# Kernel tuning notes

Hardware: AMD Instinct MI355X
Metric: run time of the kernel (lower is better)

## Reference

```python
import jax, jax.numpy as jnp
import numpy as np

B, T = 32, 50
CONCEPT_NUM = 500
C = CONCEPT_NUM + 1          # self.concept_num = concept_num + 1
H, E = 32, 32                # hidden_dim, embedding_dim
BN_SCALE = 1.0 / np.sqrt(1.0 + 1e-5)  # eval-mode BatchNorm1d, default running stats


def _mlp(x, w1, b1, w2, b2):
    # MLP: relu(fc1) -> (dropout off in eval) -> relu(fc2) -> BatchNorm1d(eval)
    x = jax.nn.relu(x @ w1.T + b1)
    x = jax.nn.relu(x @ w2.T + b2)
    return x * BN_SCALE


def _gru(x, h, w_ih, w_hh, b_ih, b_hh):
    # torch.nn.GRUCell semantics; gate order r, z, n
    gx = x @ w_ih.T + b_ih
    gh = h @ w_hh.T + b_hh
    hd = h.shape[-1]
    r = jax.nn.sigmoid(gx[..., :hd] + gh[..., :hd])
    z = jax.nn.sigmoid(gx[..., hd:2 * hd] + gh[..., hd:2 * hd])
    n = jnp.tanh(gx[..., 2 * hd:] + r * gh[..., 2 * hd:])
    return (1.0 - z) * n + z * h


def setup_inputs() -> dict:
    key = jax.random.key(0)
    ks = jax.random.split(key, 32)
    HE = H + E
    def lin(k, out_d, in_d):
        return jax.random.normal(k, (out_d, in_d), jnp.float32) * (1.0 / np.sqrt(in_d))
    inp = {
        'features': jax.random.randint(ks[0], (B, T), 0, 2 * C, jnp.int64),
        'questions': jax.random.randint(ks[1], (B, T), 0, C, jnp.int64),
        'graph': jax.random.uniform(ks[2], (C, C), jnp.float32),
        'emb_x': jax.random.normal(ks[3], (2 * C, E), jnp.float32),
        'emb_c': jax.random.normal(ks[4], (C, E), jnp.float32),
        # f_self: MLP(H+E -> H -> H)
        'self_w1': lin(ks[5], H, HE), 'self_b1': jnp.full((H,), 0.1, jnp.float32),
        'self_w2': lin(ks[6], H, H),  'self_b2': jnp.full((H,), 0.1, jnp.float32),
        # f_neighbor_list[0]: MLP(2*(H+E) -> H -> H)
        'n0_w1': lin(ks[7], H, 2 * HE), 'n0_b1': jnp.full((H,), 0.1, jnp.float32),
        'n0_w2': lin(ks[8], H, H),      'n0_b2': jnp.full((H,), 0.1, jnp.float32),
        # f_neighbor_list[1]
        'n1_w1': lin(ks[9], H, 2 * HE),  'n1_b1': jnp.full((H,), 0.1, jnp.float32),
        'n1_w2': lin(ks[10], H, H),      'n1_b2': jnp.full((H,), 0.1, jnp.float32),
        # EraseAddGate
        'ea_w': jax.random.uniform(ks[11], (C,), jnp.float32, -1.0, 1.0) / np.sqrt(C),
        'ea_ew': lin(ks[12], H, H), 'ea_eb': jnp.zeros((H,), jnp.float32),
        'ea_aw': lin(ks[13], H, H), 'ea_ab': jnp.zeros((H,), jnp.float32),
        # GRUCell
        'gru_w_ih': lin(ks[14], 3 * H, H), 'gru_w_hh': lin(ks[15], 3 * H, H),
        'gru_b_ih': jnp.zeros((3 * H,), jnp.float32), 'gru_b_hh': jnp.zeros((3 * H,), jnp.float32),
        # predict
        'pred_w': lin(ks[16], 1, H), 'pred_b': jnp.zeros((1,), jnp.float32),
    }
    return inp


def reference(features, questions, graph, emb_x, emb_c,
              self_w1, self_b1, self_w2, self_b2,
              n0_w1, n0_b1, n0_w2, n0_b2,
              n1_w1, n1_b1, n1_w2, n1_b2,
              ea_w, ea_ew, ea_eb, ea_aw, ea_ab,
              gru_w_ih, gru_w_hh, gru_b_ih, gru_b_hh,
              pred_w, pred_b):
    b_ar = jnp.arange(B)

    def step(ht, inp):
        xt, qt = inp  # [B], [B]
        # _aggregate: response embedding via one_hot(xt) @ emb_x == gather
        res_emb = emb_x[xt]                                          # [B, E]
        ce = jnp.broadcast_to(emb_c[None], (B, C, E))                # [B, C, E]
        ce = ce.at[b_ar, qt].set(res_emb)
        tmp_ht = jnp.concatenate([ht, ce], axis=-1)                  # [B, C, H+E]
        # _agg_neighbors (Dense graph, 2 edge types)
        self_ht = tmp_ht[b_ar, qt]                                   # [B, H+E]
        self_feat = _mlp(self_ht, self_w1, self_b1, self_w2, self_b2)
        neigh_ht = jnp.concatenate(
            [jnp.broadcast_to(self_ht[:, None], tmp_ht.shape), tmp_ht], axis=-1)  # [B, C, 2(H+E)]
        adj = graph[qt][..., None]                                   # [B, C, 1]
        radj = graph[:, qt].T[..., None]                             # [B, C, 1]
        neigh = adj * _mlp(neigh_ht, n0_w1, n0_b1, n0_w2, n0_b2) \
              + radj * _mlp(neigh_ht, n1_w1, n1_b1, n1_w2, n1_b2)    # [B, C, H]
        m = neigh.at[b_ar, qt].set(self_feat)
        # EraseAddGate
        eg = jax.nn.sigmoid(m @ ea_ew.T + ea_eb)
        af = jnp.tanh(m @ ea_aw.T + ea_ab)
        w = ea_w[None, :, None]
        m = m - w * eg * m + w * af
        # GRUCell over every (student, concept)
        h_next = _gru(m.reshape(-1, H), ht.reshape(-1, H),
                      gru_w_ih, gru_w_hh, gru_b_ih, gru_b_hh).reshape(B, C, H)
        yt = jax.nn.sigmoid((h_next @ pred_w.T + pred_b)[..., 0])    # [B, C]
        return h_next, yt

    ht0 = jnp.zeros((B, C, H), dtype=graph.dtype)
    _, yts = jax.lax.scan(step, ht0, (features.T, questions.T))      # [T, B, C]
    # _get_next_pred: prediction for question at t+1 from state after step t
    yts = jnp.moveaxis(yts[:-1], 0, 1)                               # [B, T-1, C]
    q_next = questions[:, 1:]                                        # [B, T-1]
    pred = jnp.take_along_axis(yts, q_next[..., None], axis=-1)[..., 0]
    return pred                                                      # [B, T-1]
```

## Files before the change

kernel.cpp:

```cpp
#include <hip/hip_runtime.h>
#include <math.h>

#define BB 32
#define TT 50
#define CC 501
#define NNODES (BB*CC)
#define BN_SCALEF 0.9999950000374996f

#define V 4
#define NPW 8
#define WPB 8
#define NTH 512
#define NPB (NPW*WPB)
#define NBLK ((NNODES + NPB - 1)/NPB)

#define HT_SZ   (NNODES*32)
#define P_SZ    (CC*32)
#define GT_SZ   (CC*CC)
#define PERB_BUF (BB*96)

__device__ __forceinline__ float dot4(float4 a, float4 b){
    return a.x*b.x + a.y*b.y + a.z*b.z + a.w*b.w;
}
__device__ __forceinline__ float sigm(float x){ return 1.f/(1.f+__expf(-x)); }
__device__ __forceinline__ float tanhfast(float x){ return 1.f - 2.f/(__expf(2.f*x)+1.f); }

__global__ void init0_kernel(const float* __restrict__ graph,
                             float* __restrict__ graphT,
                             float* __restrict__ ht) {
    int i = blockIdx.x*blockDim.x + threadIdx.x;
    if (i < HT_SZ) ht[i] = 0.f;
    if (i < GT_SZ) {
        int r = i / CC, c2 = i % CC;
        graphT[i] = graph[c2*CC + r];
    }
}

__global__ void pk_kernel(const float* __restrict__ n0_w1, const float* __restrict__ n1_w1,
                          const float* __restrict__ emb_c,
                          float* __restrict__ P0, float* __restrict__ P1) {
    int c = blockIdx.x;
    int which = threadIdx.x >> 5, j = threadIdx.x & 31;
    float ec = emb_c[c*32 + j];
    const float* W = which ? n1_w1 : n0_w1;
    float acc = 0.f;
    #pragma unroll
    for (int k = 0; k < 32; k++)
        acc += W[j*128 + 96 + k] * __shfl(ec, k, 32);
    (which ? P1 : P0)[c*32 + j] = acc;
}

__global__ void perb0_kernel(const int* __restrict__ features, const float* __restrict__ emb_x,
                             const float* __restrict__ n0_w1, const float* __restrict__ n0_b1,
                             const float* __restrict__ n1_w1, const float* __restrict__ n1_b1,
                             const float* __restrict__ self_w1, const float* __restrict__ self_b1,
                             const float* __restrict__ self_w2, const float* __restrict__ self_b2,
                             float* __restrict__ perb) {
    int b = threadIdx.x >> 5, j = threadIdx.x & 31;
    int xt = features[b*TT + 0];
    float eq = emb_x[xt*32 + j];
    float a0 = n0_b1[j], a1 = n1_b1[j], s = self_b1[j];
    #pragma unroll
    for (int k = 0; k < 32; k++) {
        float ek = __shfl(eq, k, 32);
        a0 += n0_w1[j*128 + 32 + k] * ek;
        a1 += n1_w1[j*128 + 32 + k] * ek;
        s  += self_w1[j*64 + 32 + k] * ek;
    }
    float l1 = fmaxf(s, 0.f);
    float s2 = self_b2[j];
    #pragma unroll
    for (int k = 0; k < 32; k++) s2 += self_w2[j*32 + k] * __shfl(l1, k, 32);
    perb[b*96 + j]      = a0;
    perb[b*96 + 32 + j] = a1;
    perb[b*96 + 64 + j] = fmaxf(s2, 0.f) * BN_SCALEF;
}

__global__ __launch_bounds__(NTH, 1) void step_kernel(
    int t,
    const int* __restrict__ features, const int* __restrict__ questions,
    const float* __restrict__ graph,  const float* __restrict__ emb_x,
    const float* __restrict__ self_w1, const float* __restrict__ self_b1,
    const float* __restrict__ self_w2, const float* __restrict__ self_b2,
    const float* __restrict__ n0_w1, const float* __restrict__ n0_b1,
    const float* __restrict__ n0_w2, const float* __restrict__ n0_b2,
    const float* __restrict__ n1_w1, const float* __restrict__ n1_b1,
    const float* __restrict__ n1_w2, const float* __restrict__ n1_b2,
    const float* __restrict__ ea_w,  const float* __restrict__ ea_ew,
    const float* __restrict__ ea_eb, const float* __restrict__ ea_aw,
    const float* __restrict__ ea_ab,
    const float* __restrict__ gru_w_ih, const float* __restrict__ gru_w_hh,
    const float* __restrict__ gru_b_ih, const float* __restrict__ gru_b_hh,
    const float* __restrict__ pred_w,   const float* __restrict__ pred_b,
    float* __restrict__ ht,
    const float* __restrict__ P0, const float* __restrict__ P1,
    const float* __restrict__ graphT,
    float* __restrict__ perb, float* __restrict__ out)
{
    __shared__ float Wq[12288];
    __shared__ float xb[WPB][3][NPW][32];

    int tid = threadIdx.x;
    for (int idx = tid; idx < 12288; idx += NTH) {
        float v;
        if (idx < 6144) {
            int region = idx >> 10;
            int r = idx & 1023;
            int j = (r >> 2) & 31;
            int k = ((r >> 7) << 2) | (r & 3);
            switch (region) {
                case 0:  v = n0_w1[j*128 + 64 + k]; break;
                case 1:  v = n1_w1[j*128 + 64 + k]; break;
                case 2:  v = n0_w2[j*32 + k]; break;
                case 3:  v = n1_w2[j*32 + k]; break;
                case 4:  v = ea_ew[j*32 + k]; break;
                default: v = ea_aw[j*32 + k]; break;
            }
            Wq[idx] = v;
        } else {
            int r = idx - 6144;
            int which = r / 3072;
            int r2 = r % 3072;
            int row = (r2 >> 2) % 96;
            int k = ((r2 / 384) << 2) | (r2 & 3);
            Wq[idx] = which ? gru_w_hh[row*32 + k] : gru_w_ih[row*32 + k];
        }
    }

    int l   = tid & 63;
    int w   = tid >> 6;
    int j   = l & 31, sub = l >> 5;
    int nodebase = blockIdx.x*NPB + w*NPW;
    bool act = nodebase < NNODES;

    int bv[V], cv[V], qtv[V];
    float hj[V], adjv[V], radjv[V];
    if (act) {
        #pragma unroll
        for (int v = 0; v < V; v++) {
            int node = nodebase + 2*v + sub;
            int b = node / CC;
            int c = node - b*CC;
            bv[v] = b; cv[v] = c;
            int qt = questions[b*TT + t];
            qtv[v] = qt;
            adjv[v]  = graph [qt*CC + c];
            radjv[v] = graphT[qt*CC + c];
            float h = ht[node*32 + j];
            hj[v] = h;
            xb[w][0][2*v+sub][j] = h;
        }
    }
    __syncthreads();
    if (!act) return;

    int pbase = (t & 1)*PERB_BUF;

    {
        float acc0[V], acc1[V];
        #pragma unroll
        for (int v = 0; v < V; v++) {
            acc0[v] = perb[pbase + bv[v]*96 + j]      + P0[cv[v]*32 + j];
            acc1[v] = perb[pbase + bv[v]*96 + 32 + j] + P1[cv[v]*32 + j];
        }
        #pragma unroll
        for (int kc = 0; kc < 8; kc++) {
            float4 w0 = *(const float4*)&Wq[       kc*128 + j*4];
            float4 w1 = *(const float4*)&Wq[1024 + kc*128 + j*4];
            #pragma unroll
            for (int v = 0; v < V; v++) {
                float4 x = *(const float4*)&xb[w][0][2*v+sub][kc*4];
                acc0[v] += dot4(w0, x);
                acc1[v] += dot4(w1, x);
            }
        }
        #pragma unroll
        for (int v = 0; v < V; v++) {
            xb[w][1][2*v+sub][j] = fmaxf(acc0[v], 0.f);
            xb[w][2][2*v+sub][j] = fmaxf(acc1[v], 0.f);
        }
    }

    float mval[V];
    {
        float a0[V], a1[V];
        float b0 = n0_b2[j], b1 = n1_b2[j];
        #pragma unroll
        for (int v = 0; v < V; v++) { a0[v] = b0; a1[v] = b1; }
        #pragma unroll
        for (int kc = 0; kc < 8; kc++) {
            float4 w0 = *(const float4*)&Wq[2048 + kc*128 + j*4];
            float4 w1 = *(const float4*)&Wq[3072 + kc*128 + j*4];
            #pragma unroll
            for (int v = 0; v < V; v++) {
                float4 va = *(const float4*)&xb[w][1][2*v+sub][kc*4];
                float4 vb = *(const float4*)&xb[w][2][2*v+sub][kc*4];
                a0[v] += dot4(w0, va);
                a1[v] += dot4(w1, vb);
            }
        }
        #pragma unroll
        for (int v = 0; v < V; v++) {
            float f0 = fmaxf(a0[v], 0.f) * BN_SCALEF;
            float f1 = fmaxf(a1[v], 0.f) * BN_SCALEF;
            float m = adjv[v]*f0 + radjv[v]*f1;
            if (cv[v] == qtv[v]) m = perb[pbase + bv[v]*96 + 64 + j];
            mval[v] = m;
            xb[w][1][2*v+sub][j] = m;
        }
    }

    {
        float e[V], aa[V];
        float be = ea_eb[j], ba = ea_ab[j];
        #pragma unroll
        for (int v = 0; v < V; v++) { e[v] = be; aa[v] = ba; }
        #pragma unroll
        for (int kc = 0; kc < 8; kc++) {
            float4 we = *(const float4*)&Wq[4096 + kc*128 + j*4];
            float4 wa = *(const float4*)&Wq[5120 + kc*128 + j*4];
            #pragma unroll
            for (int v = 0; v < V; v++) {
                float4 vm = *(const float4*)&xb[w][1][2*v+sub][kc*4];
                e[v]  += dot4(we, vm);
                aa[v] += dot4(wa, vm);
            }
        }
        #pragma unroll
        for (int v = 0; v < V; v++) {
            float eg = sigm(e[v]);
            float af = tanhfast(aa[v]);
            float wc = ea_w[cv[v]];
            float m  = mval[v];
            xb[w][2][2*v+sub][j] = m - wc*eg*m + wc*af;
        }
    }

    float gh0[V], gh1[V], gh2[V];
    {
        float bh0 = gru_b_hh[j], bh1 = gru_b_hh[32+j], bh2 = gru_b_hh[64+j];
        #pragma unroll
        for (int v = 0; v < V; v++) { gh0[v]=bh0; gh1[v]=bh1; gh2[v]=bh2; }
        #pragma unroll
        for (int kc = 0; kc < 8; kc++) {
            const float* wh = &Wq[9216 + kc*384];
            float4 wh0 = *(const float4*)&wh[j*4];
            float4 wh1 = *(const float4*)&wh[(32+j)*4];
            float4 wh2 = *(const float4*)&wh[(64+j)*4];
            #pragma unroll
            for (int v = 0; v < V; v++) {
                float4 vh = *(const float4*)&xb[w][0][2*v+sub][kc*4];
                gh0[v] += dot4(wh0, vh);
                gh1[v] += dot4(wh1, vh);
                gh2[v] += dot4(wh2, vh);
            }
        }
    }
    float hn[V];
    {
        float gi0[V], gi1[V], gi2[V];
        float bi0 = gru_b_ih[j], bi1 = gru_b_ih[32+j], bi2 = gru_b_ih[64+j];
        #pragma unroll
        for (int v = 0; v < V; v++) { gi0[v]=bi0; gi1[v]=bi1; gi2[v]=bi2; }
        #pragma unroll
        for (int kc = 0; kc < 8; kc++) {
            const float* wi = &Wq[6144 + kc*384];
            float4 wi0 = *(const float4*)&wi[j*4];
            float4 wi1 = *(const float4*)&wi[(32+j)*4];
            float4 wi2 = *(const float4*)&wi[(64+j)*4];
            #pragma unroll
            for (int v = 0; v < V; v++) {
                float4 vm = *(const float4*)&xb[w][2][2*v+sub][kc*4];
                gi0[v] += dot4(wi0, vm);
                gi1[v] += dot4(wi1, vm);
                gi2[v] += dot4(wi2, vm);
            }
        }
        #pragma unroll
        for (int v = 0; v < V; v++) {
            float r = sigm(gi0[v] + gh0[v]);
            float z = sigm(gi1[v] + gh1[v]);
            float n = tanhfast(gi2[v] + r*gh2[v]);
            hn[v] = (1.f - z)*n + z*hj[v];
            int node = nodebase + 2*v + sub;
            ht[node*32 + j] = hn[v];
        }
    }

    #pragma unroll
    for (int v = 0; v < V; v++) {
        int qn = questions[bv[v]*TT + t + 1];
        if (cv[v] == qn) {
            float s = hn[v] * pred_w[j];
            #pragma unroll
            for (int off = 16; off; off >>= 1) s += __shfl_down(s, off, 32);
            if (j == 0) out[bv[v]*(TT-1) + t] = sigm(s + pred_b[0]);

            if (t < TT - 2) {
                int xt1 = features[bv[v]*TT + t + 1];
                float eq = emb_x[xt1*32 + j];
                float accA0 = n0_b1[j], accA1 = n1_b1[j], accS = self_b1[j];
                #pragma unroll
                for (int k = 0; k < 32; k++) {
                    float hk = __shfl(hn[v], k, 32);
                    float ek = __shfl(eq, k, 32);
                    accA0 += n0_w1[j*128 + k]*hk + n0_w1[j*128 + 32 + k]*ek;
                    accA1 += n1_w1[j*128 + k]*hk + n1_w1[j*128 + 32 + k]*ek;
                    accS  += self_w1[j*64 + k]*hk + self_w1[j*64 + 32 + k]*ek;
                }
                float l1 = fmaxf(accS, 0.f);
                float s2 = self_b2[j];
                #pragma unroll
                for (int k = 0; k < 32; k++) s2 += self_w2[j*32 + k] * __shfl(l1, k, 32);
                float* pn = perb + ((t+1) & 1)*PERB_BUF + bv[v]*96;
                pn[j]      = accA0;
                pn[32 + j] = accA1;
                pn[64 + j] = fmaxf(s2, 0.f) * BN_SCALEF;
            }
        }
    }
}

extern "C" void kernel_launch(void* const* d_in, const int* in_sizes, int n_in,
                              void* d_out, int out_size, void* d_ws, size_t ws_size,
                              hipStream_t stream) {
    const int*   features = (const int*)  d_in[0];
    const int*   questions= (const int*)  d_in[1];
    const float* graph    = (const float*)d_in[2];
    const float* emb_x    = (const float*)d_in[3];
    const float* emb_c    = (const float*)d_in[4];
    const float* self_w1  = (const float*)d_in[5];
    const float* self_b1  = (const float*)d_in[6];
    const float* self_w2  = (const float*)d_in[7];
    const float* self_b2  = (const float*)d_in[8];
    const float* n0_w1    = (const float*)d_in[9];
    const float* n0_b1    = (const float*)d_in[10];
    const float* n0_w2    = (const float*)d_in[11];
    const float* n0_b2    = (const float*)d_in[12];
    const float* n1_w1    = (const float*)d_in[13];
    const float* n1_b1    = (const float*)d_in[14];
    const float* n1_w2    = (const float*)d_in[15];
    const float* n1_b2    = (const float*)d_in[16];
    const float* ea_w     = (const float*)d_in[17];
    const float* ea_ew    = (const float*)d_in[18];
    const float* ea_eb    = (const float*)d_in[19];
    const float* ea_aw    = (const float*)d_in[20];
    const float* ea_ab    = (const float*)d_in[21];
    const float* gru_w_ih = (const float*)d_in[22];
    const float* gru_w_hh = (const float*)d_in[23];
    const float* gru_b_ih = (const float*)d_in[24];
    const float* gru_b_hh = (const float*)d_in[25];
    const float* pred_w   = (const float*)d_in[26];
    const float* pred_b   = (const float*)d_in[27];
    float* out = (float*)d_out;

    float* ws     = (float*)d_ws;
    float* ht     = ws;
    float* P0     = ht + HT_SZ;
    float* P1     = P0 + P_SZ;
    float* graphT = P1 + P_SZ;
    float* perb   = graphT + GT_SZ;

    init0_kernel<<<(HT_SZ + 255)/256, 256, 0, stream>>>(graph, graphT, ht);
    pk_kernel<<<CC, 64, 0, stream>>>(n0_w1, n1_w1, emb_c, P0, P1);
    perb0_kernel<<<1, 1024, 0, stream>>>(features, emb_x,
        n0_w1, n0_b1, n1_w1, n1_b1, self_w1, self_b1, self_w2, self_b2, perb);

    for (int t = 0; t < TT - 1; t++) {
        step_kernel<<<NBLK, NTH, 0, stream>>>(
            t, features, questions, graph, emb_x,
            self_w1, self_b1, self_w2, self_b2,
            n0_w1, n0_b1, n0_w2, n0_b2,
            n1_w1, n1_b1, n1_w2, n1_b2,
            ea_w, ea_ew, ea_eb, ea_aw, ea_ab,
            gru_w_ih, gru_w_hh, gru_b_ih, gru_b_hh,
            pred_w, pred_b,
            ht, P0, P1, graphT, perb, out);
    }
}
```

Before: 1.225 ms.

## Fuse all timesteps into one persistent kernel with grid-wide atomic barriers

Replaces the 49 per-timestep launches with a single persistent kernel of 251 blocks that loops over timesteps and synchronises through an atomic-counter grid barrier per step. Each block loads the shared-memory weight copy once and handles its nodes in two passes, so per-step launch overhead and repeated weight staging go away. GRU hidden-gate partials are staged in shared memory to cut register pressure. It relies on all 251 blocks being co-resident, and the spin barrier adds latency and a deadlock risk if they are not.

```diff
diff --git a/kernel.cpp b/kernel.cpp
--- a/kernel.cpp
+++ b/kernel.cpp
@@ -6,19 +6,32 @@
 #define CC 501
 #define NNODES (BB*CC)
 #define BN_SCALEF 0.9999950000374996f
+#define NSTEP (TT-1)
 
 #define V 4
-#define NPW 8
-#define WPB 8
-#define NTH 512
-#define NPB (NPW*WPB)
-#define NBLK ((NNODES + NPB - 1)/NPB)
+#define WPB 4
+#define NTH 256
+#define NPB 64
+#define NBLK 251
 
 #define HT_SZ   (NNODES*32)
 #define P_SZ    (CC*32)
 #define GT_SZ   (CC*CC)
 #define PERB_BUF (BB*96)
 
+struct Params {
+    const int* features; const int* questions;
+    const float* graph;  const float* emb_x;
+    const float* self_w1; const float* self_b1; const float* self_w2; const float* self_b2;
+    const float* n0_w1; const float* n0_b1; const float* n0_w2; const float* n0_b2;
+    const float* n1_w1; const float* n1_b1; const float* n1_w2; const float* n1_b2;
+    const float* ea_w; const float* ea_ew; const float* ea_eb; const float* ea_aw; const float* ea_ab;
+    const float* gru_w_ih; const float* gru_w_hh; const float* gru_b_ih; const float* gru_b_hh;
+    const float* pred_w; const float* pred_b;
+    float* ht; const float* P0; const float* P1; const float* graphT;
+    float* perb; float* out; unsigned* bar;
+};
+
 __device__ __forceinline__ float dot4(float4 a, float4 b){
     return a.x*b.x + a.y*b.y + a.z*b.z + a.w*b.w;
 }
@@ -27,13 +40,15 @@
 
 __global__ void init0_kernel(const float* __restrict__ graph,
                              float* __restrict__ graphT,
-                             float* __restrict__ ht) {
+                             float* __restrict__ ht,
+                             unsigned* __restrict__ bar) {
     int i = blockIdx.x*blockDim.x + threadIdx.x;
     if (i < HT_SZ) ht[i] = 0.f;
     if (i < GT_SZ) {
         int r = i / CC, c2 = i % CC;
         graphT[i] = graph[c2*CC + r];
     }
+    if (i < 64) bar[i] = 0u;
 }
 
 __global__ void pk_kernel(const float* __restrict__ n0_w1, const float* __restrict__ n1_w1,
@@ -76,29 +91,23 @@
     perb[b*96 + 64 + j] = fmaxf(s2, 0.f) * BN_SCALEF;
 }
 
-__global__ __launch_bounds__(NTH, 1) void step_kernel(
-    int t,
-    const int* __restrict__ features, const int* __restrict__ questions,
-    const float* __restrict__ graph,  const float* __restrict__ emb_x,
-    const float* __restrict__ self_w1, const float* __restrict__ self_b1,
-    const float* __restrict__ self_w2, const float* __restrict__ self_b2,
-    const float* __restrict__ n0_w1, const float* __restrict__ n0_b1,
-    const float* __restrict__ n0_w2, const float* __restrict__ n0_b2,
-    const float* __restrict__ n1_w1, const float* __restrict__ n1_b1,
-    const float* __restrict__ n1_w2, const float* __restrict__ n1_b2,
-    const float* __restrict__ ea_w,  const float* __restrict__ ea_ew,
-    const float* __restrict__ ea_eb, const float* __restrict__ ea_aw,
-    const float* __restrict__ ea_ab,
-    const float* __restrict__ gru_w_ih, const float* __restrict__ gru_w_hh,
-    const float* __restrict__ gru_b_ih, const float* __restrict__ gru_b_hh,
-    const float* __restrict__ pred_w,   const float* __restrict__ pred_b,
-    float* __restrict__ ht,
-    const float* __restrict__ P0, const float* __restrict__ P1,
-    const float* __restrict__ graphT,
-    float* __restrict__ perb, float* __restrict__ out)
-{
+__device__ __forceinline__ void gbar(unsigned* ctr) {
+    __builtin_amdgcn_fence(__ATOMIC_RELEASE, "agent");
+    __syncthreads();
+    if (threadIdx.x == 0) {
+        __hip_atomic_fetch_add(ctr, 1u, __ATOMIC_RELAXED, __HIP_MEMORY_SCOPE_AGENT);
+        while (__hip_atomic_load(ctr, __ATOMIC_RELAXED, __HIP_MEMORY_SCOPE_AGENT) < (unsigned)NBLK) {
+            __builtin_amdgcn_s_sleep(2);
+        }
+    }
+    __syncthreads();
+    __builtin_amdgcn_fence(__ATOMIC_ACQUIRE, "agent");
+}
+
+__global__ __launch_bounds__(NTH, 1) void fused_kernel(Params p) {
     __shared__ float Wq[12288];
-    __shared__ float xb[WPB][3][NPW][32];
+    __shared__ float xb[WPB][3][8][32];
+    __shared__ float ghb[WPB][3][8][32];
 
     int tid = threadIdx.x;
     for (int idx = tid; idx < 12288; idx += NTH) {
@@ -106,15 +115,15 @@
         if (idx < 6144) {
             int region = idx >> 10;
             int r = idx & 1023;
-            int j = (r >> 2) & 31;
+            int jj = (r >> 2) & 31;
             int k = ((r >> 7) << 2) | (r & 3);
             switch (region) {
-                case 0:  v = n0_w1[j*128 + 64 + k]; break;
-                case 1:  v = n1_w1[j*128 + 64 + k]; break;
-                case 2:  v = n0_w2[j*32 + k]; break;
-                case 3:  v = n1_w2[j*32 + k]; break;
-                case 4:  v = ea_ew[j*32 + k]; break;
-                default: v = ea_aw[j*32 + k]; break;
+                case 0:  v = p.n0_w1[jj*128 + 64 + k]; break;
+                case 1:  v = p.n1_w1[jj*128 + 64 + k]; break;
+                case 2:  v = p.n0_w2[jj*32 + k]; break;
+                case 3:  v = p.n1_w2[jj*32 + k]; break;
+                case 4:  v = p.ea_ew[jj*32 + k]; break;
+                default: v = p.ea_aw[jj*32 + k]; break;
             }
             Wq[idx] = v;
         } else {
@@ -123,258 +132,264 @@
             int r2 = r % 3072;
             int row = (r2 >> 2) % 96;
             int k = ((r2 / 384) << 2) | (r2 & 3);
-            Wq[idx] = which ? gru_w_hh[row*32 + k] : gru_w_ih[row*32 + k];
+            Wq[idx] = which ? p.gru_w_hh[row*32 + k] : p.gru_w_ih[row*32 + k];
         }
     }
-
-    int l   = tid & 63;
-    int w   = tid >> 6;
-    int j   = l & 31, sub = l >> 5;
-    int nodebase = blockIdx.x*NPB + w*NPW;
-    bool act = nodebase < NNODES;
-
-    int bv[V], cv[V], qtv[V];
-    float hj[V], adjv[V], radjv[V];
-    if (act) {
-        #pragma unroll
-        for (int v = 0; v < V; v++) {
-            int node = nodebase + 2*v + sub;
-            int b = node / CC;
-            int c = node - b*CC;
-            bv[v] = b; cv[v] = c;
-            int qt = questions[b*TT + t];
-            qtv[v] = qt;
-            adjv[v]  = graph [qt*CC + c];
-            radjv[v] = graphT[qt*CC + c];
-            float h = ht[node*32 + j];
-            hj[v] = h;
-            xb[w][0][2*v+sub][j] = h;
-        }
-    }
     __syncthreads();
-    if (!act) return;
-
-    int pbase = (t & 1)*PERB_BUF;
-
-    {
-        float acc0[V], acc1[V];
-        #pragma unroll
-        for (int v = 0; v < V; v++) {
-            acc0[v] = perb[pbase + bv[v]*96 + j]      + P0[cv[v]*32 + j];
-            acc1[v] = perb[pbase + bv[v]*96 + 32 + j] + P1[cv[v]*32 + j];
-        }
-        #pragma unroll
-        for (int kc = 0; kc < 8; kc++) {
-            float4 w0 = *(const float4*)&Wq[       kc*128 + j*4];
-            float4 w1 = *(const float4*)&Wq[1024 + kc*128 + j*4];
-            #pragma unroll
-            for (int v = 0; v < V; v++) {
-                float4 x = *(const float4*)&xb[w][0][2*v+sub][kc*4];
-                acc0[v] += dot4(w0, x);
-                acc1[v] += dot4(w1, x);
+
+    int l = tid & 63;
+    int w = tid >> 6;
+    int j = l & 31, sub = l >> 5;
+
+    for (int t = 0; t < NSTEP; t++) {
+        int pbase = (t & 1)*PERB_BUF;
+        #pragma unroll 1
+        for (int rep = 0; rep < 2; rep++) {
+            int nodebase = blockIdx.x*NPB + rep*32 + w*8;
+            if (nodebase < NNODES) {
+                float adjv[V], radjv[V];
+                #pragma unroll
+                for (int v = 0; v < V; v++) {
+                    int node = nodebase + 2*v + sub;
+                    int b = node / CC, c = node - b*CC;
+                    int qt = p.questions[b*TT + t];
+                    adjv[v]  = p.graph [qt*CC + c];
+                    radjv[v] = p.graphT[qt*CC + c];
+                    xb[w][0][2*v+sub][j] = p.ht[node*32 + j];
+                }
+
+                {
+                    float acc0[V], acc1[V];
+                    #pragma unroll
+                    for (int v = 0; v < V; v++) {
+                        int node = nodebase + 2*v + sub;
+                        int b = node / CC, c = node - b*CC;
+                        acc0[v] = p.perb[pbase + b*96 + j]      + p.P0[c*32 + j];
+                        acc1[v] = p.perb[pbase + b*96 + 32 + j] + p.P1[c*32 + j];
+                    }
+                    #pragma unroll
+                    for (int kc = 0; kc < 8; kc++) {
+                        float4 w0 = *(const float4*)&Wq[       kc*128 + j*4];
+                        float4 w1 = *(const float4*)&Wq[1024 + kc*128 + j*4];
+                        #pragma unroll
+                        for (int v = 0; v < V; v++) {
+                            float4 x = *(const float4*)&xb[w][0][2*v+sub][kc*4];
+                            acc0[v] += dot4(w0, x);
+                            acc1[v] += dot4(w1, x);
+                        }
+                    }
+                    #pragma unroll
+                    for (int v = 0; v < V; v++) {
+                        xb[w][1][2*v+sub][j] = fmaxf(acc0[v], 0.f);
+                        xb[w][2][2*v+sub][j] = fmaxf(acc1[v], 0.f);
+                    }
+                }
+
+                {
+                    float a0[V], a1[V];
+                    float b0 = p.n0_b2[j], b1 = p.n1_b2[j];
+                    #pragma unroll
+                    for (int v = 0; v < V; v++) { a0[v] = b0; a1[v] = b1; }
+                    #pragma unroll
+                    for (int kc = 0; kc < 8; kc++) {
+                        float4 w0 = *(const float4*)&Wq[2048 + kc*128 + j*4];
+                        float4 w1 = *(const float4*)&Wq[3072 + kc*128 + j*4];
+                        #pragma unroll
+                        for (int v = 0; v < V; v++) {
+                            float4 va = *(const float4*)&xb[w][1][2*v+sub][kc*4];
+                            float4 vb = *(const float4*)&xb[w][2][2*v+sub][kc*4];
+                            a0[v] += dot4(w0, va);
+                            a1[v] += dot4(w1, vb);
+                        }
+                    }
+                    #pragma unroll
+                    for (int v = 0; v < V; v++) {
+                        int node = nodebase + 2*v + sub;
+                        int b = node / CC, c = node - b*CC;
+                        int qt = p.questions[b*TT + t];
+                        float f0 = fmaxf(a0[v], 0.f) * BN_SCALEF;
+                        float f1 = fmaxf(a1[v], 0.f) * BN_SCALEF;
+                        float m = adjv[v]*f0 + radjv[v]*f1;
+                        if (c == qt) m = p.perb[pbase + b*96 + 64 + j];
+                        xb[w][1][2*v+sub][j] = m;
+                    }
+                }
+
+                {
+                    float e[V], aa[V];
+                    float be = p.ea_eb[j], ba = p.ea_ab[j];
+                    #pragma unroll
+                    for (int v = 0; v < V; v++) { e[v] = be; aa[v] = ba; }
+                    #pragma unroll
+                    for (int kc = 0; kc < 8; kc++) {
+                        float4 we = *(const float4*)&Wq[4096 + kc*128 + j*4];
+                        float4 wa = *(const float4*)&Wq[5120 + kc*128 + j*4];
+                        #pragma unroll
+                        for (int v = 0; v < V; v++) {
+                            float4 vm = *(const float4*)&xb[w][1][2*v+sub][kc*4];
+                            e[v]  += dot4(we, vm);
+                            aa[v] += dot4(wa, vm);
+                        }
+                    }
+                    #pragma unroll
+                    for (int v = 0; v < V; v++) {
+                        int node = nodebase + 2*v + sub;
+                        int b = node / CC, c = node - b*CC;
+                        float eg = sigm(e[v]);
+                        float af = tanhfast(aa[v]);
+                        float wc = p.ea_w[c];
+                        float m  = xb[w][1][2*v+sub][j];
+                        xb[w][2][2*v+sub][j] = m - wc*eg*m + wc*af;
+                    }
+                }
+
+                {
+                    float gh0[V], gh1[V], gh2[V];
+                    float bh0 = p.gru_b_hh[j], bh1 = p.gru_b_hh[32+j], bh2 = p.gru_b_hh[64+j];
+                    #pragma unroll
+                    for (int v = 0; v < V; v++) { gh0[v]=bh0; gh1[v]=bh1; gh2[v]=bh2; }
+                    #pragma unroll
+                    for (int kc = 0; kc < 8; kc++) {
+                        const float* wh = &Wq[9216 + kc*384];
+                        float4 wh0 = *(const float4*)&wh[j*4];
+                        float4 wh1 = *(const float4*)&wh[(32+j)*4];
+                        float4 wh2 = *(const float4*)&wh[(64+j)*4];
+                        #pragma unroll
+                        for (int v = 0; v < V; v++) {
+                            float4 vh = *(const float4*)&xb[w][0][2*v+sub][kc*4];
+                            gh0[v] += dot4(wh0, vh);
+                            gh1[v] += dot4(wh1, vh);
+                            gh2[v] += dot4(wh2, vh);
+                        }
+                    }
+                    #pragma unroll
+                    for (int v = 0; v < V; v++) {
+                        ghb[w][0][2*v+sub][j] = gh0[v];
+                        ghb[w][1][2*v+sub][j] = gh1[v];
+                        ghb[w][2][2*v+sub][j] = gh2[v];
+                    }
+                }
+
+                float hn[V];
+                {
+                    float gi0[V], gi1[V], gi2[V];
+                    float bi0 = p.gru_b_ih[j], bi1 = p.gru_b_ih[32+j], bi2 = p.gru_b_ih[64+j];
+                    #pragma unroll
+                    for (int v = 0; v < V; v++) { gi0[v]=bi0; gi1[v]=bi1; gi2[v]=bi2; }
+                    #pragma unroll
+                    for (int kc = 0; kc < 8; kc++) {
+                        const float* wi = &Wq[6144 + kc*384];
+                        float4 wi0 = *(const float4*)&wi[j*4];
+                        float4 wi1 = *(const float4*)&wi[(32+j)*4];
+                        float4 wi2 = *(const float4*)&wi[(64+j)*4];
+                        #pragma unroll
+                        for (int v = 0; v < V; v++) {
+                            float4 vm = *(const float4*)&xb[w][2][2*v+sub][kc*4];
+                            gi0[v] += dot4(wi0, vm);
+                            gi1[v] += dot4(wi1, vm);
+                            gi2[v] += dot4(wi2, vm);
+                        }
+                    }
+                    #pragma unroll
+                    for (int v = 0; v < V; v++) {
+                        float hj = xb[w][0][2*v+sub][j];
+                        float r = sigm(gi0[v] + ghb[w][0][2*v+sub][j]);
+                        float z = sigm(gi1[v] + ghb[w][1][2*v+sub][j]);
+                        float n = tanhfast(gi2[v] + r*ghb[w][2][2*v+sub][j]);
+                        hn[v] = (1.f - z)*n + z*hj;
+                        int node = nodebase + 2*v + sub;
+                        p.ht[node*32 + j] = hn[v];
+                    }
+                }
+
+                #pragma unroll
+                for (int v = 0; v < V; v++) {
+                    int node = nodebase + 2*v + sub;
+                    int b = node / CC, c = node - b*CC;
+                    int qn = p.questions[b*TT + t + 1];
+                    if (c == qn) {
+                        float s = hn[v] * p.pred_w[j];
+                        #pragma unroll
+                        for (int off = 16; off; off >>= 1) s += __shfl_down(s, off, 32);
+                        if (j == 0) p.out[b*(TT-1) + t] = sigm(s + p.pred_b[0]);
+
+                        if (t < TT - 2) {
+                            int xt1 = p.features[b*TT + t + 1];
+                            float eq = p.emb_x[xt1*32 + j];
+                            float accA0 = p.n0_b1[j], accA1 = p.n1_b1[j], accS = p.self_b1[j];
+                            #pragma unroll
+                            for (int k = 0; k < 32; k++) {
+                                float hk = __shfl(hn[v], k, 32);
+                                float ek = __shfl(eq, k, 32);
+                                accA0 += p.n0_w1[j*128 + k]*hk + p.n0_w1[j*128 + 32 + k]*ek;
+                                accA1 += p.n1_w1[j*128 + k]*hk + p.n1_w1[j*128 + 32 + k]*ek;
+                                accS  += p.self_w1[j*64 + k]*hk + p.self_w1[j*64 + 32 + k]*ek;
+                            }
+                            float l1 = fmaxf(accS, 0.f);
+                            float s2 = p.self_b2[j];
+                            #pragma unroll
+                            for (int k = 0; k < 32; k++) s2 += p.self_w2[j*32 + k] * __shfl(l1, k, 32);
+                            float* pn = p.perb + ((t+1) & 1)*PERB_BUF + b*96;
+                            pn[j]      = accA0;
+                            pn[32 + j] = accA1;
+                            pn[64 + j] = fmaxf(s2, 0.f) * BN_SCALEF;
+                        }
+                    }
+                }
             }
         }
-        #pragma unroll
-        for (int v = 0; v < V; v++) {
-            xb[w][1][2*v+sub][j] = fmaxf(acc0[v], 0.f);
-            xb[w][2][2*v+sub][j] = fmaxf(acc1[v], 0.f);
-        }
-    }
-
-    float mval[V];
-    {
-        float a0[V], a1[V];
-        float b0 = n0_b2[j], b1 = n1_b2[j];
-        #pragma unroll
-        for (int v = 0; v < V; v++) { a0[v] = b0; a1[v] = b1; }
-        #pragma unroll
-        for (int kc = 0; kc < 8; kc++) {
-            float4 w0 = *(const float4*)&Wq[2048 + kc*128 + j*4];
-            float4 w1 = *(const float4*)&Wq[3072 + kc*128 + j*4];
-            #pragma unroll
-            for (int v = 0; v < V; v++) {
-                float4 va = *(const float4*)&xb[w][1][2*v+sub][kc*4];
-                float4 vb = *(const float4*)&xb[w][2][2*v+sub][kc*4];
-                a0[v] += dot4(w0, va);
-                a1[v] += dot4(w1, vb);
-            }
-        }
-        #pragma unroll
-        for (int v = 0; v < V; v++) {
-            float f0 = fmaxf(a0[v], 0.f) * BN_SCALEF;
-            float f1 = fmaxf(a1[v], 0.f) * BN_SCALEF;
-            float m = adjv[v]*f0 + radjv[v]*f1;
-            if (cv[v] == qtv[v]) m = perb[pbase + bv[v]*96 + 64 + j];
-            mval[v] = m;
-            xb[w][1][2*v+sub][j] = m;
-        }
-    }
-
-    {
-        float e[V], aa[V];
-        float be = ea_eb[j], ba = ea_ab[j];
-        #pragma unroll
-        for (int v = 0; v < V; v++) { e[v] = be; aa[v] = ba; }
-        #pragma unroll
-        for (int kc = 0; kc < 8; kc++) {
-            float4 we = *(const float4*)&Wq[4096 + kc*128 + j*4];
-            float4 wa = *(const float4*)&Wq[5120 + kc*128 + j*4];
-            #pragma unroll
-            for (int v = 0; v < V; v++) {
-                float4 vm = *(const float4*)&xb[w][1][2*v+sub][kc*4];
-                e[v]  += dot4(we, vm);
-                aa[v] += dot4(wa, vm);
-            }
-        }
-        #pragma unroll
-        for (int v = 0; v < V; v++) {
-            float eg = sigm(e[v]);
-            float af = tanhfast(aa[v]);
-            float wc = ea_w[cv[v]];
-            float m  = mval[v];
-            xb[w][2][2*v+sub][j] = m - wc*eg*m + wc*af;
-        }
-    }
-
-    float gh0[V], gh1[V], gh2[V];
-    {
-        float bh0 = gru_b_hh[j], bh1 = gru_b_hh[32+j], bh2 = gru_b_hh[64+j];
-        #pragma unroll
-        for (int v = 0; v < V; v++) { gh0[v]=bh0; gh1[v]=bh1; gh2[v]=bh2; }
-        #pragma unroll
-        for (int kc = 0; kc < 8; kc++) {
-            const float* wh = &Wq[9216 + kc*384];
-            float4 wh0 = *(const float4*)&wh[j*4];
-            float4 wh1 = *(const float4*)&wh[(32+j)*4];
-            float4 wh2 = *(const float4*)&wh[(64+j)*4];
-            #pragma unroll
-            for (int v = 0; v < V; v++) {
-                float4 vh = *(const float4*)&xb[w][0][2*v+sub][kc*4];
-                gh0[v] += dot4(wh0, vh);
-                gh1[v] += dot4(wh1, vh);
-                gh2[v] += dot4(wh2, vh);
-            }
-        }
-    }
-    float hn[V];
-    {
-        float gi0[V], gi1[V], gi2[V];
-        float bi0 = gru_b_ih[j], bi1 = gru_b_ih[32+j], bi2 = gru_b_ih[64+j];
-        #pragma unroll
-        for (int v = 0; v < V; v++) { gi0[v]=bi0; gi1[v]=bi1; gi2[v]=bi2; }
-        #pragma unroll
-        for (int kc = 0; kc < 8; kc++) {
-            const float* wi = &Wq[6144 + kc*384];
-            float4 wi0 = *(const float4*)&wi[j*4];
-            float4 wi1 = *(const float4*)&wi[(32+j)*4];
-            float4 wi2 = *(const float4*)&wi[(64+j)*4];
-            #pragma unroll
-            for (int v = 0; v < V; v++) {
-                float4 vm = *(const float4*)&xb[w][2][2*v+sub][kc*4];
-                gi0[v] += dot4(wi0, vm);
-                gi1[v] += dot4(wi1, vm);
-                gi2[v] += dot4(wi2, vm);
-            }
-        }
-        #pragma unroll
-        for (int v = 0; v < V; v++) {
-            float r = sigm(gi0[v] + gh0[v]);
-            float z = sigm(gi1[v] + gh1[v]);
-            float n = tanhfast(gi2[v] + r*gh2[v]);
-            hn[v] = (1.f - z)*n + z*hj[v];
-            int node = nodebase + 2*v + sub;
-            ht[node*32 + j] = hn[v];
-        }
-    }
-
-    #pragma unroll
-    for (int v = 0; v < V; v++) {
-        int qn = questions[bv[v]*TT + t + 1];
-        if (cv[v] == qn) {
-            float s = hn[v] * pred_w[j];
-            #pragma unroll
-            for (int off = 16; off; off >>= 1) s += __shfl_down(s, off, 32);
-            if (j == 0) out[bv[v]*(TT-1) + t] = sigm(s + pred_b[0]);
-
-            if (t < TT - 2) {
-                int xt1 = features[bv[v]*TT + t + 1];
-                float eq = emb_x[xt1*32 + j];
-                float accA0 = n0_b1[j], accA1 = n1_b1[j], accS = self_b1[j];
-                #pragma unroll
-                for (int k = 0; k < 32; k++) {
-                    float hk = __shfl(hn[v], k, 32);
-                    float ek = __shfl(eq, k, 32);
-                    accA0 += n0_w1[j*128 + k]*hk + n0_w1[j*128 + 32 + k]*ek;
-                    accA1 += n1_w1[j*128 + k]*hk + n1_w1[j*128 + 32 + k]*ek;
-                    accS  += self_w1[j*64 + k]*hk + self_w1[j*64 + 32 + k]*ek;
-                }
-                float l1 = fmaxf(accS, 0.f);
-                float s2 = self_b2[j];
-                #pragma unroll
-                for (int k = 0; k < 32; k++) s2 += self_w2[j*32 + k] * __shfl(l1, k, 32);
-                float* pn = perb + ((t+1) & 1)*PERB_BUF + bv[v]*96;
-                pn[j]      = accA0;
-                pn[32 + j] = accA1;
-                pn[64 + j] = fmaxf(s2, 0.f) * BN_SCALEF;
-            }
-        }
+        if (t != NSTEP - 1) gbar(p.bar + t);
     }
 }
 
 extern "C" void kernel_launch(void* const* d_in, const int* in_sizes, int n_in,
                               void* d_out, int out_size, void* d_ws, size_t ws_size,
                               hipStream_t stream) {
-    const int*   features = (const int*)  d_in[0];
-    const int*   questions= (const int*)  d_in[1];
-    const float* graph    = (const float*)d_in[2];
-    const float* emb_x    = (const float*)d_in[3];
-    const float* emb_c    = (const float*)d_in[4];
-    const float* self_w1  = (const float*)d_in[5];
-    const float* self_b1  = (const float*)d_in[6];
-    const float* self_w2  = (const float*)d_in[7];
-    const float* self_b2  = (const float*)d_in[8];
-    const float* n0_w1    = (const float*)d_in[9];
-    const float* n0_b1    = (const float*)d_in[10];
-    const float* n0_w2    = (const float*)d_in[11];
-    const float* n0_b2    = (const float*)d_in[12];
-    const float* n1_w1    = (const float*)d_in[13];
-    const float* n1_b1    = (const float*)d_in[14];
-    const float* n1_w2    = (const float*)d_in[15];
-    const float* n1_b2    = (const float*)d_in[16];
-    const float* ea_w     = (const float*)d_in[17];
-    const float* ea_ew    = (const float*)d_in[18];
-    const float* ea_eb    = (const float*)d_in[19];
-    const float* ea_aw    = (const float*)d_in[20];
-    const float* ea_ab    = (const float*)d_in[21];
-    const float* gru_w_ih = (const float*)d_in[22];
-    const float* gru_w_hh = (const float*)d_in[23];
-    const float* gru_b_ih = (const float*)d_in[24];
-    const float* gru_b_hh = (const float*)d_in[25];
-    const float* pred_w   = (const float*)d_in[26];
-    const float* pred_b   = (const float*)d_in[27];
-    float* out = (float*)d_out;
-
-    float* ws     = (float*)d_ws;
-    float* ht     = ws;
-    float* P0     = ht + HT_SZ;
-    float* P1     = P0 + P_SZ;
-    float* graphT = P1 + P_SZ;
-    float* perb   = graphT + GT_SZ;
-
-    init0_kernel<<<(HT_SZ + 255)/256, 256, 0, stream>>>(graph, graphT, ht);
-    pk_kernel<<<CC, 64, 0, stream>>>(n0_w1, n1_w1, emb_c, P0, P1);
-    perb0_kernel<<<1, 1024, 0, stream>>>(features, emb_x,
-        n0_w1, n0_b1, n1_w1, n1_b1, self_w1, self_b1, self_w2, self_b2, perb);
-
-    for (int t = 0; t < TT - 1; t++) {
-        step_kernel<<<NBLK, NTH, 0, stream>>>(
-            t, features, questions, graph, emb_x,
-            self_w1, self_b1, self_w2, self_b2,
-            n0_w1, n0_b1, n0_w2, n0_b2,
-            n1_w1, n1_b1, n1_w2, n1_b2,
-            ea_w, ea_ew, ea_eb, ea_aw, ea_ab,
-            gru_w_ih, gru_w_hh, gru_b_ih, gru_b_hh,
-            pred_w, pred_b,
-            ht, P0, P1, graphT, perb, out);
-    }
-}
+    Params prm;
+    prm.features = (const int*)  d_in[0];
+    prm.questions= (const int*)  d_in[1];
+    prm.graph    = (const float*)d_in[2];
+    prm.emb_x    = (const float*)d_in[3];
+    const float* emb_c = (const float*)d_in[4];
+    prm.self_w1  = (const float*)d_in[5];
+    prm.self_b1  = (const float*)d_in[6];
+    prm.self_w2  = (const float*)d_in[7];
+    prm.self_b2  = (const float*)d_in[8];
+    prm.n0_w1    = (const float*)d_in[9];
+    prm.n0_b1    = (const float*)d_in[10];
+    prm.n0_w2    = (const float*)d_in[11];
+    prm.n0_b2    = (const float*)d_in[12];
+    prm.n1_w1    = (const float*)d_in[13];
+    prm.n1_b1    = (const float*)d_in[14];
+    prm.n1_w2    = (const float*)d_in[15];
+    prm.n1_b2    = (const float*)d_in[16];
+    prm.ea_w     = (const float*)d_in[17];
+    prm.ea_ew    = (const float*)d_in[18];
+    prm.ea_eb    = (const float*)d_in[19];
+    prm.ea_aw    = (const float*)d_in[20];
+    prm.ea_ab    = (const float*)d_in[21];
+    prm.gru_w_ih = (const float*)d_in[22];
+    prm.gru_w_hh = (const float*)d_in[23];
+    prm.gru_b_ih = (const float*)d_in[24];
+    prm.gru_b_hh = (const float*)d_in[25];
+    prm.pred_w   = (const float*)d_in[26];
+    prm.pred_b   = (const float*)d_in[27];
+    prm.out = (float*)d_out;
+
+    float* ws   = (float*)d_ws;
+    prm.ht      = ws;
+    float* P0   = prm.ht + HT_SZ;
+    float* P1   = P0 + P_SZ;
+    float* gT   = P1 + P_SZ;
+    float* perb = gT + GT_SZ;
+    unsigned* bar = (unsigned*)(perb + 2*PERB_BUF);
+    prm.P0 = P0; prm.P1 = P1; prm.graphT = gT; prm.perb = perb; prm.bar = bar;
+
+    init0_kernel<<<(HT_SZ + 255)/256, 256, 0, stream>>>(prm.graph, gT, prm.ht, bar);
+    pk_kernel<<<CC, 64, 0, stream>>>(prm.n0_w1, prm.n1_w1, emb_c, P0, P1);
+    perb0_kernel<<<1, 1024, 0, stream>>>(prm.features, prm.emb_x,
+        prm.n0_w1, prm.n0_b1, prm.n1_w1, prm.n1_b1,
+        prm.self_w1, prm.self_b1, prm.self_w2, prm.self_b2, perb);
+
+    fused_kernel<<<NBLK, NTH, 0, stream>>>(prm);
+}
```

Result: slower. 2.007 ms (+63.9%).
